# Performance work log

Hardware: AMD Instinct MI355X
Metric: run time of the kernel (lower is better)

## Reference

```python
import jax, jax.numpy as jnp
import numpy as np

N, F, E, T = 50000, 128, 800000, 8


def setup_inputs() -> dict:
    key = jax.random.key(0)
    ks = jax.random.split(key, 10)
    s = 1.0 / np.sqrt(F)
    return {
        "x": jax.random.normal(ks[0], (N, F), jnp.float32),
        "edge_index": jax.random.randint(ks[1], (2, E), 0, N, jnp.int64),
        "edge_weight": jax.random.uniform(ks[2], (E,), jnp.float32),
        "W0": jax.random.normal(ks[3], (F, F), jnp.float32) * s,
        "Wih": jax.random.normal(ks[4], (3 * F, F), jnp.float32) * s,
        "Whh": jax.random.normal(ks[5], (3 * F, F), jnp.float32) * s,
        "bih": jax.random.normal(ks[6], (3 * F,), jnp.float32) * s,
        "bhh": jax.random.normal(ks[7], (3 * F,), jnp.float32) * s,
        "Wlin": jax.random.normal(ks[8], (T, F), jnp.float32) * s,
        "blin": jax.random.normal(ks[9], (T,), jnp.float32) * s,
    }


def _evolve_weight(W0, Wih, Whh, bih, bhh):
    # One GRU step with input = hidden = W0 (rows of weight matrix as batch).
    gi = W0 @ Wih.T + bih  # [F, 3F]
    gh = W0 @ Whh.T + bhh
    ir, iz, inn = jnp.split(gi, 3, axis=1)
    hr, hz, hn = jnp.split(gh, 3, axis=1)
    r = jax.nn.sigmoid(ir + hr)
    z = jax.nn.sigmoid(iz + hz)
    n = jnp.tanh(inn + r * hn)
    return (1.0 - z) * n + z * W0  # [F, F]


def reference(x, edge_index, edge_weight, W0, Wih, Whh, bih, bhh, Wlin, blin):
    n_nodes = x.shape[0]
    W = _evolve_weight(W0, Wih, Whh, bih, bhh)
    # gcn_norm with added self-loops (fill value 1.0), symmetric normalization
    loop = jnp.arange(n_nodes, dtype=edge_index.dtype)
    row = jnp.concatenate([edge_index[0], loop])
    col = jnp.concatenate([edge_index[1], loop])
    ew = jnp.concatenate([edge_weight, jnp.ones((n_nodes,), edge_weight.dtype)])
    deg = jax.ops.segment_sum(ew, col, num_segments=n_nodes)
    dinv = jnp.where(deg > 0, jax.lax.rsqrt(jnp.where(deg > 0, deg, 1.0)), 0.0)
    norm = dinv[row] * ew * dinv[col]  # [E+N]
    xw = x @ W  # [N, F]
    h = jax.ops.segment_sum(norm[:, None] * xw[row], col, num_segments=n_nodes)
    h = jax.nn.relu(h)
    return h @ Wlin.T + blin  # [N, n_target]
```

## Files before the change

kernel.cpp:

```cpp
#include <hip/hip_runtime.h>
#include <math.h>

#define F 128
#define FIX18     262144.0f
#define INV18     (1.0f / 262144.0f)
#define EVB 256
#define CAP 48

using bf16x8 = __attribute__((ext_vector_type(8))) short;
using f32x4  = __attribute__((ext_vector_type(4))) float;

__device__ inline int read_idx(const int* ei, long long elem, int i64) {
    return i64 ? (int)((const long long*)ei)[elem] : ei[elem];
}
__device__ inline unsigned int f2bf_rn(float f) {
    unsigned int b = __float_as_uint(f);
    return (b + 0x7FFFu + ((b >> 16) & 1u)) >> 16;
}
__device__ inline float bflo(unsigned int u) { return __uint_as_float(u << 16); }
__device__ inline float bfhi(unsigned int u) { return __uint_as_float(u & 0xFFFF0000u); }

__device__ inline void acc8(float* acc, float wt, uint4 v) {
    acc[0] += wt * bflo(v.x); acc[1] += wt * bfhi(v.x);
    acc[2] += wt * bflo(v.y); acc[3] += wt * bfhi(v.y);
    acc[4] += wt * bflo(v.z); acc[5] += wt * bfhi(v.z);
    acc[6] += wt * bflo(v.w); acc[7] += wt * bfhi(v.w);
}

__device__ inline float dinv_of(unsigned int c32) {
    return rsqrtf(1.0f + (float)(c32 & 0xFFFFFFu) * INV18);
}

__device__ inline int detect_i64(const int* ei) {
    int lane = threadIdx.x & 63;
    int hi = ei[2 * (lane & 31) + 1];
    unsigned long long m = __ballot(hi != 0);
    return m == 0ULL;
}

__global__ __launch_bounds__(256) void k_evolve_bucket(
        const int* __restrict__ ei, const float* __restrict__ ew,
        unsigned int* __restrict__ cnt32, int2* __restrict__ ep,
        int E, int N,
        const float* __restrict__ W0, const float* __restrict__ Wih,
        const float* __restrict__ Whh, const float* __restrict__ bih,
        const float* __restrict__ bhh,
        unsigned short* __restrict__ Wth, unsigned short* __restrict__ Wtl) {
    int b = (int)blockIdx.x;
    if (b >= EVB) {
        int i64 = detect_i64(ei);
        int base = (b - EVB) * 1024 + threadIdx.x;
        #pragma unroll
        for (int u = 0; u < 4; ++u) {
            int e = base + u * 256;
            if (e < E) {
                int r = read_idx(ei, e, i64);
                int c = read_idx(ei, (long long)E + e, i64);
                float w = ew[e];
                unsigned int uu = (1u << 24) | (unsigned int)(w * FIX18 + 0.5f);
                unsigned int old = atomicAdd(&cnt32[c], uu);
                unsigned int slot = old >> 24;
                if (slot < CAP)
                    ep[(size_t)c * CAP + slot] = make_int2(r, __float_as_int(w));
            }
        }
        return;
    }
    int wave = threadIdx.x >> 6, lane = threadIdx.x & 63;
    int gw = b * 4 + wave;
    int pairBase = gw * 16;
    int i = pairBase >> 7;
    int jb = pairBase & 127;
    int lp = lane & 15, sl = lane >> 4;
    int j = jb + lp;
    const float* w0p = W0 + (size_t)i * F;
    const float* pir = Wih + (size_t)j * F;
    const float* piz = Wih + (size_t)(j + F) * F;
    const float* pin = Wih + (size_t)(j + 2 * F) * F;
    const float* phr = Whh + (size_t)j * F;
    const float* phz = Whh + (size_t)(j + F) * F;
    const float* phn = Whh + (size_t)(j + 2 * F) * F;
    float air = 0, aiz = 0, ain = 0, ahr = 0, ahz = 0, ahn = 0;
    int k0 = sl * 32;
    #pragma unroll
    for (int kk = 0; kk < 32; kk += 4) {
        int k = k0 + kk;
        float4 w0 = *(const float4*)&w0p[k];
        float4 a;
        a = *(const float4*)&pir[k]; air += w0.x*a.x + w0.y*a.y + w0.z*a.z + w0.w*a.w;
        a = *(const float4*)&piz[k]; aiz += w0.x*a.x + w0.y*a.y + w0.z*a.z + w0.w*a.w;
        a = *(const float4*)&pin[k]; ain += w0.x*a.x + w0.y*a.y + w0.z*a.z + w0.w*a.w;
        a = *(const float4*)&phr[k]; ahr += w0.x*a.x + w0.y*a.y + w0.z*a.z + w0.w*a.w;
        a = *(const float4*)&phz[k]; ahz += w0.x*a.x + w0.y*a.y + w0.z*a.z + w0.w*a.w;
        a = *(const float4*)&phn[k]; ahn += w0.x*a.x + w0.y*a.y + w0.z*a.z + w0.w*a.w;
    }
    air += __shfl_xor(air, 16, 64); air += __shfl_xor(air, 32, 64);
    aiz += __shfl_xor(aiz, 16, 64); aiz += __shfl_xor(aiz, 32, 64);
    ain += __shfl_xor(ain, 16, 64); ain += __shfl_xor(ain, 32, 64);
    ahr += __shfl_xor(ahr, 16, 64); ahr += __shfl_xor(ahr, 32, 64);
    ahz += __shfl_xor(ahz, 16, 64); ahz += __shfl_xor(ahz, 32, 64);
    ahn += __shfl_xor(ahn, 16, 64); ahn += __shfl_xor(ahn, 32, 64);
    if (sl == 0) {
        air += bih[j];          ahr += bhh[j];
        aiz += bih[j + F];      ahz += bhh[j + F];
        ain += bih[j + 2 * F];  ahn += bhh[j + 2 * F];
        float r = 1.0f / (1.0f + expf(-(air + ahr)));
        float z = 1.0f / (1.0f + expf(-(aiz + ahz)));
        float n = tanhf(ain + r * ahn);
        float w = (1.0f - z) * n + z * w0p[j];
        unsigned int hb = f2bf_rn(w);
        float whi = __uint_as_float(hb << 16);
        unsigned int lb = f2bf_rn(w - whi);
        Wth[j * F + i] = (unsigned short)hb;
        Wtl[j * F + i] = (unsigned short)lb;
    }
}

__global__ __launch_bounds__(256) void k_cast(
        const float2* __restrict__ x2, const unsigned int* __restrict__ cnt32,
        unsigned int* __restrict__ xs, int M) {
    int id = blockIdx.x * 256 + threadIdx.x;
    if (id >= M) return;
    float di = dinv_of(cnt32[id >> 6]);
    float2 v = x2[id];
    xs[id] = f2bf_rn(di * v.x) | (f2bf_rn(di * v.y) << 16);
}

__global__ __launch_bounds__(256) void k_agg2(const uint4* __restrict__ xs4,
                                              const unsigned int* __restrict__ cnt32,
                                              const int2* __restrict__ ep,
                                              uint4* __restrict__ hagg4, int N) {
    int wave = threadIdx.x >> 6, lane = threadIdx.x & 63;
    int c = blockIdx.x * 4 + wave;
    if (c >= N) return;
    int g = lane >> 4, sl = lane & 15;
    unsigned int pc = cnt32[c];
    int cnt = (int)(pc >> 24); if (cnt > CAP) cnt = CAP;
    float di = dinv_of(pc);
    int start = c * CAP, end = start + cnt;
    float a0[8] = {0,0,0,0,0,0,0,0}, a1[8] = {0,0,0,0,0,0,0,0};
    if (g == 0) {
        uint4 v = xs4[(size_t)c * 16 + sl];
        a0[0] = bflo(v.x); a0[1] = bfhi(v.x);
        a0[2] = bflo(v.y); a0[3] = bfhi(v.y);
        a0[4] = bflo(v.z); a0[5] = bfhi(v.z);
        a0[6] = bflo(v.w); a0[7] = bfhi(v.w);
    }
    int last = end - 1;
    for (int k = start; k < end; k += 16) {
        int iA = k + g, iB = k + g + 4, iC = k + g + 8, iD = k + g + 12;
        int2 eA = ep[min(iA, last)];
        int2 eB = ep[min(iB, last)];
        int2 eC = ep[min(iC, last)];
        int2 eD = ep[min(iD, last)];
        uint4 vA = xs4[(size_t)eA.x * 16 + sl];
        uint4 vB = xs4[(size_t)eB.x * 16 + sl];
        uint4 vC = xs4[(size_t)eC.x * 16 + sl];
        uint4 vD = xs4[(size_t)eD.x * 16 + sl];
        float wA = (iA <= last) ? __int_as_float(eA.y) : 0.f;
        float wB = (iB <= last) ? __int_as_float(eB.y) : 0.f;
        float wC = (iC <= last) ? __int_as_float(eC.y) : 0.f;
        float wD = (iD <= last) ? __int_as_float(eD.y) : 0.f;
        acc8(a0, wA, vA);
        acc8(a1, wB, vB);
        acc8(a0, wC, vC);
        acc8(a1, wD, vD);
    }
    #pragma unroll
    for (int f = 0; f < 8; ++f) {
        float v = a0[f] + a1[f];
        v += __shfl_xor(v, 16, 64);
        v += __shfl_xor(v, 32, 64);
        a0[f] = v;
    }
    if (lane < 16) {
        uint4 o;
        o.x = f2bf_rn(di * a0[0]) | (f2bf_rn(di * a0[1]) << 16);
        o.y = f2bf_rn(di * a0[2]) | (f2bf_rn(di * a0[3]) << 16);
        o.z = f2bf_rn(di * a0[4]) | (f2bf_rn(di * a0[5]) << 16);
        o.w = f2bf_rn(di * a0[6]) | (f2bf_rn(di * a0[7]) << 16);
        hagg4[(size_t)c * 16 + lane] = o;
    }
}

__global__ __launch_bounds__(256) void k_gemm(const uint4* __restrict__ hagg4,
                                              const unsigned short* __restrict__ Wth,
                                              const unsigned short* __restrict__ Wtl,
                                              const float* __restrict__ Wlin,
                                              const float* __restrict__ blin,
                                              float* __restrict__ out, int N) {
    __shared__ __align__(16) unsigned int At[64 * 68];
    __shared__ __align__(16) float WlinL[8 * F];
    int t = threadIdx.x;
    int row0 = blockIdx.x * 64;
    #pragma unroll
    for (int it = 0; it < 4; ++it) {
        int idx = it * 256 + t;
        int rr = idx >> 4, c4 = idx & 15;
        uint4 v = make_uint4(0u, 0u, 0u, 0u);
        if (row0 + rr < N) v = hagg4[(size_t)(row0 + rr) * 16 + c4];
        *(uint4*)&At[rr * 68 + c4 * 4] = v;
    }
    *(float4*)&WlinL[t * 4] = *(const float4*)&Wlin[t * 4];
    __syncthreads();

    int wave = t >> 6, lane = t & 63;
    int sl = lane & 15, q = lane >> 4;
    const unsigned short* Ash = (const unsigned short*)At;
    int mrow = wave * 16 + sl;

    f32x4 acc[8];
    #pragma unroll
    for (int nt = 0; nt < 8; ++nt) acc[nt] = (f32x4){0.f, 0.f, 0.f, 0.f};
    #pragma unroll
    for (int ko = 0; ko < 4; ++ko) {
        bf16x8 a = *(const bf16x8*)&Ash[mrow * 136 + ko * 32 + q * 8];
        #pragma unroll
        for (int nt = 0; nt < 8; ++nt) {
            int boff = (nt * 16 + sl) * F + ko * 32 + q * 8;
            bf16x8 bh = *(const bf16x8*)&Wth[boff];
            bf16x8 bl = *(const bf16x8*)&Wtl[boff];
            acc[nt] = __builtin_amdgcn_mfma_f32_16x16x32_bf16(a, bh, acc[nt], 0, 0, 0);
            acc[nt] = __builtin_amdgcn_mfma_f32_16x16x32_bf16(a, bl, acc[nt], 0, 0, 0);
        }
    }
    #pragma unroll
    for (int nt = 0; nt < 8; ++nt)
        #pragma unroll
        for (int r = 0; r < 4; ++r) acc[nt][r] = fmaxf(acc[nt][r], 0.f);

    float p[8][4];
    #pragma unroll
    for (int tt = 0; tt < 8; ++tt) {
        float wl[8];
        #pragma unroll
        for (int nt = 0; nt < 8; ++nt) wl[nt] = WlinL[tt * F + nt * 16 + sl];
        #pragma unroll
        for (int r = 0; r < 4; ++r) {
            float s = 0.f;
            #pragma unroll
            for (int nt = 0; nt < 8; ++nt) s += acc[nt][r] * wl[nt];
            p[tt][r] = s;
        }
    }
    #pragma unroll
    for (int tt = 0; tt < 8; ++tt)
        #pragma unroll
        for (int r = 0; r < 4; ++r) {
            float v = p[tt][r];
            v += __shfl_xor(v, 1, 64); v += __shfl_xor(v, 2, 64);
            v += __shfl_xor(v, 4, 64); v += __shfl_xor(v, 8, 64);
            p[tt][r] = v;
        }
    if (sl == 0) {
        #pragma unroll
        for (int r = 0; r < 4; ++r) {
            int row = row0 + wave * 16 + q * 4 + r;
            if (row < N) {
                #pragma unroll
                for (int tt = 0; tt < 8; ++tt)
                    out[(size_t)row * 8 + tt] = p[tt][r] + blin[tt];
            }
        }
    }
}

extern "C" void kernel_launch(void* const* d_in, const int* in_sizes, int n_in,
                              void* d_out, int out_size, void* d_ws, size_t ws_size,
                              hipStream_t stream) {
    const float* x    = (const float*)d_in[0];
    const int*   ei   = (const int*)d_in[1];
    const float* ew   = (const float*)d_in[2];
    const float* W0   = (const float*)d_in[3];
    const float* Wih  = (const float*)d_in[4];
    const float* Whh  = (const float*)d_in[5];
    const float* bih  = (const float*)d_in[6];
    const float* bhh  = (const float*)d_in[7];
    const float* Wlin = (const float*)d_in[8];
    const float* blin = (const float*)d_in[9];
    int N = in_sizes[0] / F;
    int E = in_sizes[1] / 2;
    float* outp = (float*)d_out;

    int cntBlocks4 = (E + 1023) / 1024;
    int M = N * 64;

    char* wsb = (char*)d_ws;
    size_t cur = 0;
    auto alloc = [&](size_t sz) -> void* {
        void* p = wsb + cur;
        cur = (cur + sz + 255) & ~(size_t)255;
        return p;
    };
    unsigned int* cnt32 = (unsigned int*)alloc((size_t)N * 4);
    int2*  ep   = (int2*) alloc((size_t)N * CAP * 8);
    unsigned short* Wth = (unsigned short*)alloc((size_t)F * F * 2);
    unsigned short* Wtl = (unsigned short*)alloc((size_t)F * F * 2);
    unsigned int* xs    = (unsigned int*)alloc((size_t)N * 64 * 4);
    unsigned int* hagg  = (unsigned int*)alloc((size_t)N * 64 * 4);
    (void)ws_size; (void)n_in; (void)out_size;

    hipMemsetAsync(cnt32, 0, (size_t)N * 4, stream);
    hipLaunchKernelGGL(k_evolve_bucket, dim3(EVB + cntBlocks4), dim3(256), 0, stream,
                       ei, ew, cnt32, ep, E, N,
                       W0, Wih, Whh, bih, bhh, Wth, Wtl);
    hipLaunchKernelGGL(k_cast, dim3((M + 255) / 256), dim3(256), 0, stream,
                       (const float2*)x, cnt32, xs, M);
    hipLaunchKernelGGL(k_agg2, dim3((N + 3) / 4), dim3(256), 0, stream,
                       (const uint4*)xs, cnt32, ep, (uint4*)hagg, N);
    hipLaunchKernelGGL(k_gemm, dim3((N + 63) / 64), dim3(256), 0, stream,
                       (const uint4*)hagg, Wth, Wtl, Wlin, blin, outp, N);
}
```

Before: 200.6 us.

## Privatize per-node edge counters into eight copies to reduce atomic contention

Splits the per-destination atomic counter and edge bucket into eight copies selected by block index, so concurrent blocks rarely hit the same counter. Downstream kernels sum the eight weight fields for the degree normalization, and the aggregation kernel maps a flat edge index across the eight sub-buckets. This enlarges the bucket buffer and memset and adds per-edge slot-mapping arithmetic and extra counter reads in exchange for less atomic serialization.

```diff
diff --git a/kernel.cpp b/kernel.cpp
--- a/kernel.cpp
+++ b/kernel.cpp
@@ -5,7 +5,8 @@
 #define FIX18     262144.0f
 #define INV18     (1.0f / 262144.0f)
 #define EVB 256
-#define CAP 48
+#define NCPY 8
+#define CAP8 16
 
 using bf16x8 = __attribute__((ext_vector_type(8))) short;
 using f32x4  = __attribute__((ext_vector_type(4))) float;
@@ -27,10 +28,6 @@
     acc[6] += wt * bflo(v.w); acc[7] += wt * bfhi(v.w);
 }
 
-__device__ inline float dinv_of(unsigned int c32) {
-    return rsqrtf(1.0f + (float)(c32 & 0xFFFFFFu) * INV18);
-}
-
 __device__ inline int detect_i64(const int* ei) {
     int lane = threadIdx.x & 63;
     int hi = ei[2 * (lane & 31) + 1];
@@ -38,9 +35,21 @@
     return m == 0ULL;
 }
 
+__device__ inline int map_slot(int t, const int* cnt) {
+    int pos = t, k = 0, alive = 1;
+    #pragma unroll
+    for (int kk = 0; kk < 7; ++kk) {
+        int cond = alive & (pos >= cnt[kk]);
+        pos -= cond ? cnt[kk] : 0;
+        k += cond;
+        alive = cond;
+    }
+    return k * CAP8 + pos;
+}
+
 __global__ __launch_bounds__(256) void k_evolve_bucket(
         const int* __restrict__ ei, const float* __restrict__ ew,
-        unsigned int* __restrict__ cnt32, int2* __restrict__ ep,
+        unsigned int* __restrict__ cnt8, int2* __restrict__ ep,
         int E, int N,
         const float* __restrict__ W0, const float* __restrict__ Wih,
         const float* __restrict__ Whh, const float* __restrict__ bih,
@@ -50,6 +59,8 @@
     if (b >= EVB) {
         int i64 = detect_i64(ei);
         int base = (b - EVB) * 1024 + threadIdx.x;
+        unsigned int copy = b & (NCPY - 1);
+        unsigned int* pk = cnt8 + (size_t)copy * N;
         #pragma unroll
         for (int u = 0; u < 4; ++u) {
             int e = base + u * 256;
@@ -58,10 +69,11 @@
                 int c = read_idx(ei, (long long)E + e, i64);
                 float w = ew[e];
                 unsigned int uu = (1u << 24) | (unsigned int)(w * FIX18 + 0.5f);
-                unsigned int old = atomicAdd(&cnt32[c], uu);
+                unsigned int old = atomicAdd(&pk[c], uu);
                 unsigned int slot = old >> 24;
-                if (slot < CAP)
-                    ep[(size_t)c * CAP + slot] = make_int2(r, __float_as_int(w));
+                if (slot < CAP8)
+                    ep[((size_t)c * NCPY + copy) * CAP8 + slot] =
+                        make_int2(r, __float_as_int(w));
             }
         }
         return;
@@ -117,27 +129,39 @@
 }
 
 __global__ __launch_bounds__(256) void k_cast(
-        const float2* __restrict__ x2, const unsigned int* __restrict__ cnt32,
-        unsigned int* __restrict__ xs, int M) {
+        const float2* __restrict__ x2, const unsigned int* __restrict__ cnt8,
+        unsigned int* __restrict__ xs, int M, int N) {
     int id = blockIdx.x * 256 + threadIdx.x;
     if (id >= M) return;
-    float di = dinv_of(cnt32[id >> 6]);
+    int node = id >> 6;
+    unsigned int wsum = 0;
+    #pragma unroll
+    for (int k = 0; k < NCPY; ++k) wsum += cnt8[(size_t)k * N + node] & 0xFFFFFFu;
+    float di = rsqrtf(1.0f + (float)wsum * INV18);
     float2 v = x2[id];
     xs[id] = f2bf_rn(di * v.x) | (f2bf_rn(di * v.y) << 16);
 }
 
 __global__ __launch_bounds__(256) void k_agg2(const uint4* __restrict__ xs4,
-                                              const unsigned int* __restrict__ cnt32,
+                                              const unsigned int* __restrict__ cnt8,
                                               const int2* __restrict__ ep,
                                               uint4* __restrict__ hagg4, int N) {
     int wave = threadIdx.x >> 6, lane = threadIdx.x & 63;
     int c = blockIdx.x * 4 + wave;
     if (c >= N) return;
     int g = lane >> 4, sl = lane & 15;
-    unsigned int pc = cnt32[c];
-    int cnt = (int)(pc >> 24); if (cnt > CAP) cnt = CAP;
-    float di = dinv_of(pc);
-    int start = c * CAP, end = start + cnt;
+    int cnt[NCPY];
+    unsigned int wsum = 0;
+    int total = 0;
+    #pragma unroll
+    for (int k = 0; k < NCPY; ++k) {
+        unsigned int p = cnt8[(size_t)k * N + c];
+        int ck = (int)(p >> 24); if (ck > CAP8) ck = CAP8;
+        cnt[k] = ck; total += ck;
+        wsum += p & 0xFFFFFFu;
+    }
+    float di = rsqrtf(1.0f + (float)wsum * INV18);
+    const int2* epc = ep + (size_t)c * NCPY * CAP8;
     float a0[8] = {0,0,0,0,0,0,0,0}, a1[8] = {0,0,0,0,0,0,0,0};
     if (g == 0) {
         uint4 v = xs4[(size_t)c * 16 + sl];
@@ -146,21 +170,21 @@
         a0[4] = bflo(v.z); a0[5] = bfhi(v.z);
         a0[6] = bflo(v.w); a0[7] = bfhi(v.w);
     }
-    int last = end - 1;
-    for (int k = start; k < end; k += 16) {
-        int iA = k + g, iB = k + g + 4, iC = k + g + 8, iD = k + g + 12;
-        int2 eA = ep[min(iA, last)];
-        int2 eB = ep[min(iB, last)];
-        int2 eC = ep[min(iC, last)];
-        int2 eD = ep[min(iD, last)];
+    int last = total - 1;
+    for (int t0 = 0; t0 < total; t0 += 16) {
+        int tA = t0 + g, tB = t0 + g + 4, tC = t0 + g + 8, tD = t0 + g + 12;
+        int2 eA = epc[map_slot(min(tA, last), cnt)];
+        int2 eB = epc[map_slot(min(tB, last), cnt)];
+        int2 eC = epc[map_slot(min(tC, last), cnt)];
+        int2 eD = epc[map_slot(min(tD, last), cnt)];
         uint4 vA = xs4[(size_t)eA.x * 16 + sl];
         uint4 vB = xs4[(size_t)eB.x * 16 + sl];
         uint4 vC = xs4[(size_t)eC.x * 16 + sl];
         uint4 vD = xs4[(size_t)eD.x * 16 + sl];
-        float wA = (iA <= last) ? __int_as_float(eA.y) : 0.f;
-        float wB = (iB <= last) ? __int_as_float(eB.y) : 0.f;
-        float wC = (iC <= last) ? __int_as_float(eC.y) : 0.f;
-        float wD = (iD <= last) ? __int_as_float(eD.y) : 0.f;
+        float wA = (tA <= last) ? __int_as_float(eA.y) : 0.f;
+        float wB = (tB <= last) ? __int_as_float(eB.y) : 0.f;
+        float wC = (tC <= last) ? __int_as_float(eC.y) : 0.f;
+        float wD = (tD <= last) ? __int_as_float(eD.y) : 0.f;
         acc8(a0, wA, vA);
         acc8(a1, wB, vB);
         acc8(a0, wC, vC);
@@ -292,22 +316,22 @@
         cur = (cur + sz + 255) & ~(size_t)255;
         return p;
     };
-    unsigned int* cnt32 = (unsigned int*)alloc((size_t)N * 4);
-    int2*  ep   = (int2*) alloc((size_t)N * CAP * 8);
+    unsigned int* cnt8 = (unsigned int*)alloc((size_t)N * NCPY * 4);
+    int2*  ep   = (int2*) alloc((size_t)N * NCPY * CAP8 * 8);
     unsigned short* Wth = (unsigned short*)alloc((size_t)F * F * 2);
     unsigned short* Wtl = (unsigned short*)alloc((size_t)F * F * 2);
     unsigned int* xs    = (unsigned int*)alloc((size_t)N * 64 * 4);
     unsigned int* hagg  = (unsigned int*)alloc((size_t)N * 64 * 4);
     (void)ws_size; (void)n_in; (void)out_size;
 
-    hipMemsetAsync(cnt32, 0, (size_t)N * 4, stream);
+    hipMemsetAsync(cnt8, 0, (size_t)N * NCPY * 4, stream);
     hipLaunchKernelGGL(k_evolve_bucket, dim3(EVB + cntBlocks4), dim3(256), 0, stream,
-                       ei, ew, cnt32, ep, E, N,
+                       ei, ew, cnt8, ep, E, N,
                        W0, Wih, Whh, bih, bhh, Wth, Wtl);
     hipLaunchKernelGGL(k_cast, dim3((M + 255) / 256), dim3(256), 0, stream,
-                       (const float2*)x, cnt32, xs, M);
+                       (const float2*)x, cnt8, xs, M, N);
     hipLaunchKernelGGL(k_agg2, dim3((N + 3) / 4), dim3(256), 0, stream,
-                       (const uint4*)xs, cnt32, ep, (uint4*)hagg, N);
+                       (const uint4*)xs, cnt8, ep, (uint4*)hagg, N);
     hipLaunchKernelGGL(k_gemm, dim3((N + 63) / 64), dim3(256), 0, stream,
                        (const uint4*)hagg, Wth, Wtl, Wlin, blin, outp, N);
 }
```

Measured after the change: 216.8 us. +8.1%, slower.

## Fuse x cast into bucket kernel and apply source dinv during aggregation

Applied to the files above, without the earlier changes.

The separate cast kernel is removed. The x-to-bf16 conversion now runs as extra blocks of the evolve/bucket kernel and no longer needs the finished degree counts. To allow this, the source-side dinv scaling moves into the aggregation loop, where an extra gather of cnt32[row] per edge supplies it, and the self-loop term is scaled by di. This saves one launch and lets the cast overlap with the atomic bucketing, at the cost of an extra scattered 4-byte load per edge in the gather kernel and bf16 rounding of unscaled x.

```diff
diff --git a/kernel.cpp b/kernel.cpp
--- a/kernel.cpp
+++ b/kernel.cpp
@@ -38,15 +38,23 @@
     return m == 0ULL;
 }
 
-__global__ __launch_bounds__(256) void k_evolve_bucket(
+__global__ __launch_bounds__(256) void k_evolve_bucket_cast(
         const int* __restrict__ ei, const float* __restrict__ ew,
         unsigned int* __restrict__ cnt32, int2* __restrict__ ep,
-        int E, int N,
+        int E, int N, int cntBlocks4,
         const float* __restrict__ W0, const float* __restrict__ Wih,
         const float* __restrict__ Whh, const float* __restrict__ bih,
         const float* __restrict__ bhh,
-        unsigned short* __restrict__ Wth, unsigned short* __restrict__ Wtl) {
+        unsigned short* __restrict__ Wth, unsigned short* __restrict__ Wtl,
+        const float2* __restrict__ x2, unsigned int* __restrict__ xs, int M) {
     int b = (int)blockIdx.x;
+    if (b >= EVB + cntBlocks4) {
+        int id = (b - EVB - cntBlocks4) * 256 + threadIdx.x;
+        if (id >= M) return;
+        float2 v = x2[id];
+        xs[id] = f2bf_rn(v.x) | (f2bf_rn(v.y) << 16);
+        return;
+    }
     if (b >= EVB) {
         int i64 = detect_i64(ei);
         int base = (b - EVB) * 1024 + threadIdx.x;
@@ -116,16 +124,6 @@
     }
 }
 
-__global__ __launch_bounds__(256) void k_cast(
-        const float2* __restrict__ x2, const unsigned int* __restrict__ cnt32,
-        unsigned int* __restrict__ xs, int M) {
-    int id = blockIdx.x * 256 + threadIdx.x;
-    if (id >= M) return;
-    float di = dinv_of(cnt32[id >> 6]);
-    float2 v = x2[id];
-    xs[id] = f2bf_rn(di * v.x) | (f2bf_rn(di * v.y) << 16);
-}
-
 __global__ __launch_bounds__(256) void k_agg2(const uint4* __restrict__ xs4,
                                               const unsigned int* __restrict__ cnt32,
                                               const int2* __restrict__ ep,
@@ -141,10 +139,7 @@
     float a0[8] = {0,0,0,0,0,0,0,0}, a1[8] = {0,0,0,0,0,0,0,0};
     if (g == 0) {
         uint4 v = xs4[(size_t)c * 16 + sl];
-        a0[0] = bflo(v.x); a0[1] = bfhi(v.x);
-        a0[2] = bflo(v.y); a0[3] = bfhi(v.y);
-        a0[4] = bflo(v.z); a0[5] = bfhi(v.z);
-        a0[6] = bflo(v.w); a0[7] = bfhi(v.w);
+        acc8(a0, di, v);
     }
     int last = end - 1;
     for (int k = start; k < end; k += 16) {
@@ -157,10 +152,10 @@
         uint4 vB = xs4[(size_t)eB.x * 16 + sl];
         uint4 vC = xs4[(size_t)eC.x * 16 + sl];
         uint4 vD = xs4[(size_t)eD.x * 16 + sl];
-        float wA = (iA <= last) ? __int_as_float(eA.y) : 0.f;
-        float wB = (iB <= last) ? __int_as_float(eB.y) : 0.f;
-        float wC = (iC <= last) ? __int_as_float(eC.y) : 0.f;
-        float wD = (iD <= last) ? __int_as_float(eD.y) : 0.f;
+        float wA = (iA <= last) ? __int_as_float(eA.y) * dinv_of(cnt32[eA.x]) : 0.f;
+        float wB = (iB <= last) ? __int_as_float(eB.y) * dinv_of(cnt32[eB.x]) : 0.f;
+        float wC = (iC <= last) ? __int_as_float(eC.y) * dinv_of(cnt32[eC.x]) : 0.f;
+        float wD = (iD <= last) ? __int_as_float(eD.y) * dinv_of(cnt32[eD.x]) : 0.f;
         acc8(a0, wA, vA);
         acc8(a1, wB, vB);
         acc8(a0, wC, vC);
@@ -284,6 +279,7 @@
 
     int cntBlocks4 = (E + 1023) / 1024;
     int M = N * 64;
+    int castBlocks = (M + 255) / 256;
 
     char* wsb = (char*)d_ws;
     size_t cur = 0;
@@ -301,11 +297,10 @@
     (void)ws_size; (void)n_in; (void)out_size;
 
     hipMemsetAsync(cnt32, 0, (size_t)N * 4, stream);
-    hipLaunchKernelGGL(k_evolve_bucket, dim3(EVB + cntBlocks4), dim3(256), 0, stream,
-                       ei, ew, cnt32, ep, E, N,
-                       W0, Wih, Whh, bih, bhh, Wth, Wtl);
-    hipLaunchKernelGGL(k_cast, dim3((M + 255) / 256), dim3(256), 0, stream,
-                       (const float2*)x, cnt32, xs, M);
+    hipLaunchKernelGGL(k_evolve_bucket_cast, dim3(EVB + cntBlocks4 + castBlocks), dim3(256), 0, stream,
+                       ei, ew, cnt32, ep, E, N, cntBlocks4,
+                       W0, Wih, Whh, bih, bhh, Wth, Wtl,
+                       (const float2*)x, xs, M);
     hipLaunchKernelGGL(k_agg2, dim3((N + 3) / 4), dim3(256), 0, stream,
                        (const uint4*)xs, cnt32, ep, (uint4*)hagg, N);
     hipLaunchKernelGGL(k_gemm, dim3((N + 63) / 64), dim3(256), 0, stream,
```

New measurement: 207.5 us. 1.03x slower.
